# Kernel optimization log

Hardware: AMD Instinct MI355X
Metric: run time of the kernel (lower is better)

## Reference

```python
import jax, jax.numpy as jnp
import numpy as np

NUM_BANDS = 30
SPLIT_FREQ = 30
M_PARAM = 1
DIM = 2048
BATCH = 16384


def _dct_mat(N):
    # Orthonormal DCT-II matrix D: dct(x) = x @ D.T, idct(y) = y @ D
    n = np.arange(N, dtype=np.float64)
    kk = n[:, None]
    M = np.cos(np.pi * (n + 0.5) * kk / N)
    s = np.full(N, np.sqrt(2.0 / N))
    s[0] = np.sqrt(1.0 / N)
    return jnp.asarray((M * s[:, None]).astype(np.float32))


def _band_scale(freq_weights, k, N):
    # Precompute the per-frequency scale vector the torch loop applies band-by-band.
    pts = np.linspace(0, N - 1, NUM_BANDS + 1).astype(np.int64)  # torch .long() truncation
    scale = jnp.ones((N,), dtype=freq_weights.dtype)
    for i in range(NUM_BANDS):
        s, e = int(pts[i]), int(pts[i + 1])
        if e <= SPLIT_FREQ:
            f = 1.0 + freq_weights[i] * k * (1.0 - i / NUM_BANDS)
        else:
            f = 1.0 - freq_weights[i] * k * (1.0 - (i - NUM_BANDS // M_PARAM) / NUM_BANDS)
        scale = scale.at[s:e].set(f)  # bands are disjoint; base is 1
    return scale


def setup_inputs() -> dict:
    key = jax.random.key(0)
    ks = jax.random.split(key, 6)
    g = 0.02  # small init like xavier_uniform with gain 0.5
    return {
        "x": jax.random.normal(ks[0], (BATCH, DIM), dtype=jnp.float32),
        "freq_weights": jnp.ones((NUM_BANDS,), dtype=jnp.float32),
        "k": jnp.float32(0.3),
        "W1": jax.random.normal(ks[1], (1024, DIM), dtype=jnp.float32) * g,
        "b1": jnp.zeros((1024,), dtype=jnp.float32),
        "W2": jax.random.normal(ks[2], (512, 1024), dtype=jnp.float32) * g,
        "b2": jnp.zeros((512,), dtype=jnp.float32),
        "Wmu": jax.random.normal(ks[3], (256, 512), dtype=jnp.float32) * g,
        "bmu": jnp.zeros((256,), dtype=jnp.float32),
        "Wlv": jax.random.normal(ks[4], (256, 512), dtype=jnp.float32) * g,
        "blv": jnp.zeros((256,), dtype=jnp.float32),
    }


def reference(x, freq_weights, k, W1, b1, W2, b2, Wmu, bmu, Wlv, blv):
    N = x.shape[-1]
    D = _dct_mat(N)
    # DCT -> per-band reweight -> IDCT, fused as two matmuls and one vector multiply
    xd = (x @ D.T) * _band_scale(freq_weights, k, N)
    xe = xd @ D
    h = jax.nn.relu(xe @ W1.T + b1)
    h = jax.nn.relu(h @ W2.T + b2)
    mu = h @ Wmu.T + bmu
    logvar = h @ Wlv.T + blv
    return (mu, logvar)
```

## Files before the change

### kernel.cpp

```cpp
#include <hip/hip_runtime.h>
#include <hip/hip_bf16.h>
#include <math.h>

#define DIM 2048
#define BATCH 16384

typedef __attribute__((ext_vector_type(8))) short short8;
typedef __attribute__((ext_vector_type(4))) short short4v;
typedef __attribute__((ext_vector_type(4))) float floatx4;
typedef unsigned short ushort_t;

__device__ __forceinline__ ushort_t f2bf(float f) {
    union { float f; unsigned u; } v; v.f = f;
    unsigned r = v.u + 0x7FFFu + ((v.u >> 16) & 1u);
    return (ushort_t)(r >> 16);
}

__global__ void k_scale(const float* __restrict__ fw, const float* __restrict__ kp,
                        float* __restrict__ s) {
    int n = blockIdx.x * blockDim.x + threadIdx.x;
    if (n >= DIM) return;
    float kv = kp[0];
    float f = 1.0f;
    for (int i = 0; i < 30; ++i) {
        long s0 = (long)((double)i       * (double)(DIM - 1) / 30.0);
        long e0 = (long)((double)(i + 1) * (double)(DIM - 1) / 30.0);
        if (n >= s0 && n < e0) {
            if (e0 <= 30)
                f = 1.0f + fw[i] * kv * (1.0f - (float)i / 30.0f);
            else
                f = 1.0f - fw[i] * kv * (1.0f - (float)(i - 30) / 30.0f);
        }
    }
    s[n] = f;
}

__global__ void k_gen_d(ushort_t* __restrict__ D, ushort_t* __restrict__ Dt) {
    int idx = blockIdx.x * blockDim.x + threadIdx.x;
    int r = idx >> 11;
    int c = idx & (DIM - 1);
    const float w  = 7.6699039394282058e-4f;
    const float s0 = 0.02209708691207961f;
    const float s1 = 0.03125f;
    int m1 = ((2 * c + 1) * r) & (4 * DIM - 1);
    int m2 = ((2 * r + 1) * c) & (4 * DIM - 1);
    float v1 = __cosf(w * (float)m1) * (r == 0 ? s0 : s1);
    float v2 = __cosf(w * (float)m2) * (c == 0 ? s0 : s1);
    D[idx]  = f2bf(v1);
    Dt[idx] = f2bf(v2);
}

#define U_W1   262144
#define U_W2    65536
#define U_WH    16384
__global__ void k_cast_w(const float* __restrict__ W1, const float* __restrict__ W2,
                         const float* __restrict__ Wmu, const float* __restrict__ Wlv,
                         ushort_t* __restrict__ W1bf, ushort_t* __restrict__ W2bf,
                         ushort_t* __restrict__ Wcat) {
    int i = blockIdx.x * blockDim.x + threadIdx.x;
    const float* src; ushort_t* dst; int u;
    if (i < U_W1)                    { src = W1;  dst = W1bf;             u = i; }
    else if (i < U_W1 + U_W2)        { src = W2;  dst = W2bf;             u = i - U_W1; }
    else if (i < U_W1 + U_W2 + U_WH) { src = Wmu; dst = Wcat;             u = i - U_W1 - U_W2; }
    else                             { src = Wlv; dst = Wcat + 8 * U_WH;  u = i - U_W1 - U_W2 - U_WH; }
    const float4* p = reinterpret_cast<const float4*>(src) + 2 * (size_t)u;
    float4 a = p[0], b = p[1];
    short8 r;
    r[0] = (short)f2bf(a.x); r[1] = (short)f2bf(a.y);
    r[2] = (short)f2bf(a.z); r[3] = (short)f2bf(a.w);
    r[4] = (short)f2bf(b.x); r[5] = (short)f2bf(b.y);
    r[6] = (short)f2bf(b.z); r[7] = (short)f2bf(b.w);
    *reinterpret_cast<short8*>(dst + 8 * (size_t)u) = r;
}

__global__ void k_red(const float* __restrict__ P, ushort_t* __restrict__ out,
                      const float* __restrict__ scale, int n4, int n4row) {
    int i = blockIdx.x * blockDim.x + threadIdx.x;
    const float4* p = reinterpret_cast<const float4*>(P);
    float4 a = p[i], b = p[i + n4], c = p[i + 2 * n4], d = p[i + 3 * n4];
    float4 s;
    s.x = a.x + b.x + c.x + d.x;
    s.y = a.y + b.y + c.y + d.y;
    s.z = a.z + b.z + c.z + d.z;
    s.w = a.w + b.w + c.w + d.w;
    if (scale) {
        float4 sc = reinterpret_cast<const float4*>(scale)[i & (n4row - 1)];
        s.x *= sc.x; s.y *= sc.y; s.z *= sc.z; s.w *= sc.w;
    }
    short4v o;
    o[0] = (short)f2bf(s.x); o[1] = (short)f2bf(s.y);
    o[2] = (short)f2bf(s.z); o[3] = (short)f2bf(s.w);
    *reinterpret_cast<short4v*>(out + 4 * (size_t)i) = o;
}

template<int TM, int TN, int BK, int EPI, bool SK4>
__device__ __forceinline__ void gemm_core(
        const ushort_t* __restrict__ A, const ushort_t* __restrict__ B,
        ushort_t* __restrict__ Cb, float* __restrict__ Cf,
        const float* __restrict__ ep0, const float* __restrict__ ep1,
        int M, int N, int K, int KC) {
    constexpr int BM = 32 * TM;
    constexpr int BN = 32 * TN;
    constexpr int SEGS = BK / 8;
    constexpr int RSH  = (BK == 32) ? 1 : 0;
    constexpr int SSH  = (SEGS == 4) ? 2 : 3;
    __shared__ __align__(16) ushort_t As[BM * BK];
    __shared__ __align__(16) ushort_t Bs[BN * BK];

    const int tid  = threadIdx.x;
    const int lane = tid & 63;
    const int wave = tid >> 6;
    const int wm   = wave >> 1;
    const int wn   = wave & 1;
    const int q    = lane >> 4;
    const int l16  = lane & 15;

    const int tilesM = M / BM;
    const int tilesN = N / BN;
    int bid = (int)blockIdx.x;
    int sk = 0;
    if constexpr (SK4) { int nt = tilesM * tilesN; sk = bid / nt; bid = bid % nt; }
    const int xcd = bid & 7;
    const int j   = bid >> 3;
    const int bm  = xcd * (tilesM >> 3) + j / tilesN;
    const int bn  = j % tilesN;

    floatx4 acc[TM][TN];
    #pragma unroll
    for (int i = 0; i < TM; ++i)
        #pragma unroll
        for (int jj = 0; jj < TN; ++jj)
            acc[i][jj] = (floatx4){0.f, 0.f, 0.f, 0.f};

    const long aBase = (long)bm * BM * K + (long)sk * KC;
    const long bBase = (long)bn * BN * K + (long)sk * KC;
    const int  KLOOP = SK4 ? KC : K;

    for (int kt = 0; kt < KLOOP; kt += BK) {
        __syncthreads();
        #pragma unroll
        for (int i = 0; i < BM * BK / 2048; ++i) {
            int idx = tid + i * 256;
            int row = idx >> SSH, seg = idx & (SEGS - 1);
            int gseg = seg ^ ((row >> RSH) & (SEGS - 1));
            const ushort_t* g = A + aBase + (long)row * K + kt + gseg * 8;
            __builtin_amdgcn_global_load_lds(
                (const __attribute__((address_space(1))) void*)g,
                (__attribute__((address_space(3))) void*)(As + idx * 8),
                16, 0, 0);
        }
        #pragma unroll
        for (int i = 0; i < BN * BK / 2048; ++i) {
            int idx = tid + i * 256;
            int row = idx >> SSH, seg = idx & (SEGS - 1);
            int gseg = seg ^ ((row >> RSH) & (SEGS - 1));
            const ushort_t* g = B + bBase + (long)row * K + kt + gseg * 8;
            __builtin_amdgcn_global_load_lds(
                (const __attribute__((address_space(1))) void*)g,
                (__attribute__((address_space(3))) void*)(Bs + idx * 8),
                16, 0, 0);
        }
        __syncthreads();

        #pragma unroll
        for (int ks = 0; ks < BK / 32; ++ks) {
            short8 af[TM], bfr[TN];
            #pragma unroll
            for (int t = 0; t < TM; ++t) {
                int srow = wm * TM * 16 + t * 16 + l16;
                int rseg = (ks * 4 + q) ^ ((srow >> RSH) & (SEGS - 1));
                af[t] = *reinterpret_cast<const short8*>(&As[srow * BK + rseg * 8]);
            }
            #pragma unroll
            for (int t = 0; t < TN; ++t) {
                int srow = wn * TN * 16 + t * 16 + l16;
                int rseg = (ks * 4 + q) ^ ((srow >> RSH) & (SEGS - 1));
                bfr[t] = *reinterpret_cast<const short8*>(&Bs[srow * BK + rseg * 8]);
            }
            #pragma unroll
            for (int i = 0; i < TM; ++i)
                #pragma unroll
                for (int jj = 0; jj < TN; ++jj)
                    acc[i][jj] = __builtin_amdgcn_mfma_f32_16x16x32_bf16(
                        af[i], bfr[jj], acc[i][jj], 0, 0, 0);
        }
    }

    #pragma unroll
    for (int i = 0; i < TM; ++i) {
        #pragma unroll
        for (int jj = 0; jj < TN; ++jj) {
            #pragma unroll
            for (int r = 0; r < 4; ++r) {
                int row = bm * BM + wm * TM * 16 + i * 16 + q * 4 + r;
                int col = bn * BN + wn * TN * 16 + jj * 16 + l16;
                float v = acc[i][jj][r];
                if constexpr (EPI == 2) {
                    v += ep0[col];
                    v = v > 0.f ? v : 0.f;
                    Cb[(long)row * N + col] = f2bf(v);
                } else if constexpr (EPI == 3) {
                    const int half = N >> 1;
                    if (col < half)
                        Cf[(long)row * half + col] = v + ep0[col];
                    else
                        Cf[(long)M * half + (long)row * half + (col - half)] = v + ep1[col - half];
                } else {
                    Cf[(long)sk * M * N + (long)row * N + col] = v;
                }
            }
        }
    }
}

__global__ __launch_bounds__(512, 2) void g2f(const float* __restrict__ Xf,
        const ushort_t* __restrict__ B, ushort_t* __restrict__ Cb,
        const float* __restrict__ bias, int M, int N, int K) {
    constexpr int BM = 256, BN = 256, BK = 32;
    __shared__ __align__(16) ushort_t As[4][BM * BK];
    __shared__ __align__(16) ushort_t Bs[4][BN * BK];

    const int tid  = threadIdx.x;
    const int lane = tid & 63;
    const int wave = tid >> 6;
    const int wm   = wave >> 2;
    const int wn   = wave & 3;
    const int q    = lane >> 4;
    const int l16  = lane & 15;

    const int tilesM = M / BM;
    const int tilesN = N / BN;
    int bid = (int)blockIdx.x;
    const int xcd = bid & 7;
    const int jb  = bid >> 3;
    const int bm  = xcd * (tilesM >> 3) + jb / tilesN;
    const int bn  = jb % tilesN;
    const int NT  = K / BK;

    const long aBase = (long)bm * BM * K;
    const long bBase = (long)bn * BN * K;

    floatx4 acc[8][4];
    #pragma unroll
    for (int i = 0; i < 8; ++i)
        #pragma unroll
        for (int j = 0; j < 4; ++j)
            acc[i][j] = (floatx4){0.f, 0.f, 0.f, 0.f};

    float4 rAa[4], rAb[4];

#define LDA(tt, RA) do {                                                            \
        _Pragma("unroll")                                                           \
        for (int _g = 0; _g < 2; ++_g) {                                            \
            int _idx = _g * 512 + tid;                                              \
            int _row = _idx >> 2, _seg = _idx & 3;                                  \
            int _gs = _seg ^ ((_row >> 1) & 3);                                     \
            const float4* _p = reinterpret_cast<const float4*>(                     \
                Xf + aBase + (long)_row * K + (tt) * BK + _gs * 8);                 \
            RA[2 * _g]     = _p[0];                                                 \
            RA[2 * _g + 1] = _p[1];                                                 \
        } } while (0)

#define CVW(tt, RA) do { const int _sl = (tt) & 3;                                  \
        _Pragma("unroll")                                                           \
        for (int _g = 0; _g < 2; ++_g) {                                            \
            int _idx = _g * 512 + tid;                                              \
            float4 _a = RA[2 * _g], _b = RA[2 * _g + 1];                            \
            short8 _o;                                                              \
            _o[0] = (short)f2bf(_a.x); _o[1] = (short)f2bf(_a.y);                   \
            _o[2] = (short)f2bf(_a.z); _o[3] = (short)f2bf(_a.w);                   \
            _o[4] = (short)f2bf(_b.x); _o[5] = (short)f2bf(_b.y);                   \
            _o[6] = (short)f2bf(_b.z); _o[7] = (short)f2bf(_b.w);                   \
            *reinterpret_cast<short8*>(&As[_sl][_idx * 8]) = _o;                    \
        } } while (0)

#define STG_B(tt) do { const int _sl = (tt) & 3;                                    \
        _Pragma("unroll")                                                           \
        for (int _g = 0; _g < 2; ++_g) {                                            \
            int _idx = _g * 512 + tid;                                              \
            int _row = _idx >> 2, _seg = _idx & 3;                                  \
            int _gs = _seg ^ ((_row >> 1) & 3);                                     \
            const ushort_t* _gp = B + bBase + (long)_row * K + (tt) * BK + _gs * 8; \
            __builtin_amdgcn_global_load_lds(                                       \
                (const __attribute__((address_space(1))) void*)_gp,                 \
                (__attribute__((address_space(3))) void*)(&Bs[_sl][_idx * 8]),      \
                16, 0, 0);                                                          \
        } } while (0)

#define ITER(tt, RA) do {                                                           \
        const int _slot = (tt) & 3;                                                 \
        if ((tt) + 2 < NT) CVW((tt) + 2, RA);                                       \
        short8 _bf[4], _alo[4], _ahi[4];                                            \
        _Pragma("unroll")                                                           \
        for (int _j = 0; _j < 4; ++_j) {                                            \
            int _sr = wn * 64 + _j * 16 + l16;                                      \
            int _rs = q ^ ((_sr >> 1) & 3);                                         \
            _bf[_j] = *reinterpret_cast<const short8*>(&Bs[_slot][_sr * BK + _rs * 8]); \
        }                                                                           \
        _Pragma("unroll")                                                           \
        for (int _i = 0; _i < 4; ++_i) {                                            \
            int _sr = wm * 128 + _i * 16 + l16;                                     \
            int _rs = q ^ ((_sr >> 1) & 3);                                         \
            _alo[_i] = *reinterpret_cast<const short8*>(&As[_slot][_sr * BK + _rs * 8]); \
        }                                                                           \
        _Pragma("unroll")                                                           \
        for (int _i = 0; _i < 4; ++_i) {                                            \
            int _sr = wm * 128 + 64 + _i * 16 + l16;                                \
            int _rs = q ^ ((_sr >> 1) & 3);                                         \
            _ahi[_i] = *reinterpret_cast<const short8*>(&As[_slot][_sr * BK + _rs * 8]); \
        }                                                                           \
        if ((tt) + 3 < NT) STG_B((tt) + 3);                                         \
        if ((tt) + 4 < NT) LDA((tt) + 4, RA);                                       \
        __builtin_amdgcn_s_setprio(1);                                              \
        _Pragma("unroll")                                                           \
        for (int _i = 0; _i < 4; ++_i)                                              \
            _Pragma("unroll")                                                       \
            for (int _j = 0; _j < 4; ++_j)                                          \
                acc[_i][_j] = __builtin_amdgcn_mfma_f32_16x16x32_bf16(              \
                    _alo[_i], _bf[_j], acc[_i][_j], 0, 0, 0);                       \
        _Pragma("unroll")                                                           \
        for (int _i = 0; _i < 4; ++_i)                                              \
            _Pragma("unroll")                                                       \
            for (int _j = 0; _j < 4; ++_j)                                          \
                acc[4 + _i][_j] = __builtin_amdgcn_mfma_f32_16x16x32_bf16(          \
                    _ahi[_i], _bf[_j], acc[4 + _i][_j], 0, 0, 0);                   \
        __builtin_amdgcn_s_setprio(0);                                              \
        asm volatile("s_waitcnt lgkmcnt(0)" ::: "memory");                          \
        __builtin_amdgcn_sched_barrier(0);                                          \
        if ((tt) == NT - 2)                                                         \
            asm volatile("s_waitcnt vmcnt(0)" ::: "memory");                        \
        __builtin_amdgcn_s_barrier();                                               \
        asm volatile("" ::: "memory");                                              \
    } while (0)

    LDA(0, rAa); CVW(0, rAa);
    LDA(1, rAb); CVW(1, rAb);
    LDA(2, rAa); LDA(3, rAb);
    STG_B(0); STG_B(1); STG_B(2);
    asm volatile("s_waitcnt lgkmcnt(0)" ::: "memory");
    asm volatile("s_waitcnt vmcnt(4)" ::: "memory");
    __builtin_amdgcn_s_barrier();
    asm volatile("" ::: "memory");

    for (int t = 0; t < NT; t += 2) {
        ITER(t, rAa);
        ITER(t + 1, rAb);
    }

#undef ITER
#undef STG_B
#undef CVW
#undef LDA

    float bsv[4];
    #pragma unroll
    for (int j = 0; j < 4; ++j)
        bsv[j] = bias[bn * BN + wn * 64 + j * 16 + l16];
    #pragma unroll
    for (int i = 0; i < 8; ++i) {
        int row = bm * BM + wm * 128 + i * 16 + q * 4;
        #pragma unroll
        for (int j = 0; j < 4; ++j) {
            int col = bn * BN + wn * 64 + j * 16 + l16;
            #pragma unroll
            for (int r = 0; r < 4; ++r) {
                float v = acc[i][j][r] + bsv[j];
                v = v > 0.f ? v : 0.f;
                Cb[(long)(row + r) * N + col] = f2bf(v);
            }
        }
    }
}

template<int EPI>
__device__ __forceinline__ void gemm128_v2(
        const ushort_t* __restrict__ A, const ushort_t* __restrict__ B,
        ushort_t* __restrict__ Cb, float* __restrict__ Cf,
        const float* __restrict__ ep0, const float* __restrict__ ep1,
        int M, int N, int K) {
    constexpr int BM = 128, BN = 128, BK = 32;
    __shared__ __align__(16) ushort_t As[4][BM * BK];
    __shared__ __align__(16) ushort_t Bs[4][BN * BK];

    const int tid  = threadIdx.x;
    const int lane = tid & 63;
    const int wave = tid >> 6;
    const int wm   = wave >> 1;
    const int wn   = wave & 1;
    const int q    = lane >> 4;
    const int l16  = lane & 15;

    const int tilesM = M / BM;
    const int tilesN = N / BN;
    int bid = (int)blockIdx.x;
    const int xcd = bid & 7;
    const int jb  = bid >> 3;
    const int bm  = xcd * (tilesM >> 3) + jb / tilesN;
    const int bn  = jb % tilesN;
    const int NT  = K / BK;

    const long aBase = (long)bm * BM * K;
    const long bBase = (long)bn * BN * K;

    floatx4 acc[4][4];
    #pragma unroll
    for (int i = 0; i < 4; ++i)
        #pragma unroll
        for (int j = 0; j < 4; ++j)
            acc[i][j] = (floatx4){0.f, 0.f, 0.f, 0.f};

#define STAGE_A(t) do { int _sl = (t) & 3;                                          \
        _Pragma("unroll")                                                           \
        for (int _g = 0; _g < 2; ++_g) {                                            \
            int _idx = _g * 256 + tid;                                              \
            int _row = _idx >> 2, _seg = _idx & 3;                                  \
            int _gs = _seg ^ ((_row >> 1) & 3);                                     \
            const ushort_t* _gp = A + aBase + (long)_row * K + (t) * BK + _gs * 8;  \
            __builtin_amdgcn_global_load_lds(                                       \
                (const __attribute__((address_space(1))) void*)_gp,                 \
                (__attribute__((address_space(3))) void*)(&As[_sl][_idx * 8]),      \
                16, 0, 0);                                                          \
        } } while (0)
#define STAGE_B(t) do { int _sl = (t) & 3;                                          \
        _Pragma("unroll")                                                           \
        for (int _g = 0; _g < 2; ++_g) {                                            \
            int _idx = _g * 256 + tid;                                              \
            int _row = _idx >> 2, _seg = _idx & 3;                                  \
            int _gs = _seg ^ ((_row >> 1) & 3);                                     \
            const ushort_t* _gp = B + bBase + (long)_row * K + (t) * BK + _gs * 8;  \
            __builtin_amdgcn_global_load_lds(                                       \
                (const __attribute__((address_space(1))) void*)_gp,                 \
                (__attribute__((address_space(3))) void*)(&Bs[_sl][_idx * 8]),      \
                16, 0, 0);                                                          \
        } } while (0)

    STAGE_A(0); STAGE_B(0);
    STAGE_A(1); STAGE_B(1);
    STAGE_A(2); STAGE_B(2);
    asm volatile("s_waitcnt vmcnt(8)" ::: "memory");
    __builtin_amdgcn_s_barrier();
    asm volatile("" ::: "memory");

#define KTILE(tt, DOSTAGE, WAITOP) do {                                             \
        const int _slot = (tt) & 3;                                                 \
        short8 _bf[4], _af[4];                                                      \
        _Pragma("unroll")                                                           \
        for (int _j = 0; _j < 4; ++_j) {                                            \
            int _sr = wn * 64 + _j * 16 + l16;                                      \
            int _rs = q ^ ((_sr >> 1) & 3);                                         \
            _bf[_j] = *reinterpret_cast<const short8*>(&Bs[_slot][_sr * BK + _rs * 8]); \
        }                                                                           \
        _Pragma("unroll")                                                           \
        for (int _i = 0; _i < 4; ++_i) {                                            \
            int _sr = wm * 64 + _i * 16 + l16;                                      \
            int _rs = q ^ ((_sr >> 1) & 3);                                         \
            _af[_i] = *reinterpret_cast<const short8*>(&As[_slot][_sr * BK + _rs * 8]); \
        }                                                                           \
        if (DOSTAGE) { STAGE_A((tt) + 3); STAGE_B((tt) + 3); }                      \
        __builtin_amdgcn_s_setprio(1);                                              \
        _Pragma("unroll")                                                           \
        for (int _i = 0; _i < 4; ++_i)                                              \
            _Pragma("unroll")                                                       \
            for (int _j = 0; _j < 4; ++_j)                                          \
                acc[_i][_j] = __builtin_amdgcn_mfma_f32_16x16x32_bf16(              \
                    _af[_i], _bf[_j], acc[_i][_j], 0, 0, 0);                        \
        __builtin_amdgcn_s_setprio(0);                                              \
        asm volatile("s_waitcnt lgkmcnt(0)" ::: "memory");                          \
        __builtin_amdgcn_sched_barrier(0);                                          \
        WAITOP;                                                                     \
        __builtin_amdgcn_s_barrier();                                               \
        asm volatile("" ::: "memory");                                              \
    } while (0)

    int t = 0;
    for (; t < NT - 3; ++t) {
        KTILE(t, true, asm volatile("s_waitcnt vmcnt(8)" ::: "memory"));
    }
    KTILE(t, false, asm volatile("s_waitcnt vmcnt(4)" ::: "memory")); ++t;
    KTILE(t, false, asm volatile("s_waitcnt vmcnt(0)" ::: "memory")); ++t;
    KTILE(t, false, (void)0);

#undef KTILE
#undef STAGE_A
#undef STAGE_B

    #pragma unroll
    for (int i = 0; i < 4; ++i) {
        #pragma unroll
        for (int jj = 0; jj < 4; ++jj) {
            #pragma unroll
            for (int r = 0; r < 4; ++r) {
                int row = bm * BM + wm * 64 + i * 16 + q * 4 + r;
                int col = bn * BN + wn * 64 + jj * 16 + l16;
                float v = acc[i][jj][r];
                if constexpr (EPI == 2) {
                    v += ep0[col];
                    v = v > 0.f ? v : 0.f;
                    Cb[(long)row * N + col] = f2bf(v);
                } else {
                    const int half = N >> 1;
                    v += (col < half) ? ep0[col] : ep1[col - half];
                    if (col < half)
                        Cf[(long)row * half + col] = v;
                    else
                        Cf[(long)M * half + (long)row * half + (col - half)] = v;
                }
            }
        }
    }
}

__global__ __launch_bounds__(256) void g0p_sk(const ushort_t* A, const ushort_t* B,
        float* P, int M, int N, int K, int KC) {
    gemm_core<4, 4, 32, 4, true>(A, B, nullptr, P, nullptr, nullptr, M, N, K, KC);
}
__global__ __launch_bounds__(256) void g1p_sk(const ushort_t* A, const ushort_t* B,
        float* P, int M, int N, int K, int KC) {
    gemm_core<4, 4, 32, 4, true>(A, B, nullptr, P, nullptr, nullptr, M, N, K, KC);
}
__global__ __launch_bounds__(256, 2) void g3_h2(const ushort_t* A, const ushort_t* B,
        ushort_t* Cb, const float* ep0, int M, int N, int K) {
    gemm128_v2<2>(A, B, Cb, nullptr, ep0, nullptr, M, N, K);
}
__global__ __launch_bounds__(256, 2) void g4_head(const ushort_t* A, const ushort_t* B,
        float* Cf, const float* ep0, const float* ep1, int M, int N, int K) {
    gemm128_v2<3>(A, B, nullptr, Cf, ep0, ep1, M, N, K);
}

extern "C" void kernel_launch(void* const* d_in, const int* in_sizes, int n_in,
                              void* d_out, int out_size, void* d_ws, size_t ws_size,
                              hipStream_t stream) {
    const float* x   = (const float*)d_in[0];
    const float* fw  = (const float*)d_in[1];
    const float* kp  = (const float*)d_in[2];
    const float* W1  = (const float*)d_in[3];
    const float* b1  = (const float*)d_in[4];
    const float* W2  = (const float*)d_in[5];
    const float* b2  = (const float*)d_in[6];
    const float* Wmu = (const float*)d_in[7];
    const float* bmu = (const float*)d_in[8];
    const float* Wlv = (const float*)d_in[9];
    const float* blv = (const float*)d_in[10];
    float* out = (float*)d_out;

    char* ws = (char*)d_ws;
    const size_t MB = 1024 * 1024;
    ushort_t* W1bf = (ushort_t*)(ws + 0);
    ushort_t* Dbf  = (ushort_t*)(ws + 4   * MB);
    ushort_t* Dtbf = (ushort_t*)(ws + 12  * MB);
    ushort_t* T1sT = (ushort_t*)(ws + 20  * MB);
    ushort_t* H1   = (ushort_t*)(ws + 0);
    float*    P    = (float*)   (ws + 32  * MB);
    ushort_t* H2   = (ushort_t*)(ws + 96  * MB);
    ushort_t* M1T  = (ushort_t*)(ws + 112 * MB);
    ushort_t* W2bf = (ushort_t*)(ws + 116 * MB);
    ushort_t* Wcat = (ushort_t*)(ws + 117 * MB);
    float*    svec = (float*)   (ws + 118 * MB);

    hipLaunchKernelGGL(k_scale, dim3(DIM / 256), dim3(256), 0, stream, fw, kp, svec);
    hipLaunchKernelGGL(k_gen_d, dim3(DIM * DIM / 256), dim3(256), 0, stream, Dbf, Dtbf);
    hipLaunchKernelGGL(k_cast_w, dim3((U_W1 + U_W2 + 2 * U_WH) / 256), dim3(256), 0, stream,
                       W1, W2, Wmu, Wlv, W1bf, W2bf, Wcat);

    hipLaunchKernelGGL(g0p_sk, dim3(8 * 16 * 4), dim3(256), 0, stream,
                       W1bf, Dbf, P, 1024, 2048, 2048, 512);
    hipLaunchKernelGGL(k_red, dim3(1024 * 2048 / 4 / 256), dim3(256), 0, stream,
                       P, T1sT, svec, 1024 * 2048 / 4, 2048 / 4);
    hipLaunchKernelGGL(g1p_sk, dim3(8 * 16 * 4), dim3(256), 0, stream,
                       T1sT, Dtbf, P, 1024, 2048, 2048, 512);
    hipLaunchKernelGGL(k_red, dim3(1024 * 2048 / 4 / 256), dim3(256), 0, stream,
                       P, M1T, nullptr, 1024 * 2048 / 4, 2048 / 4);

    hipLaunchKernelGGL(g2f, dim3((BATCH / 256) * (1024 / 256)), dim3(512), 0, stream,
                       x, M1T, H1, b1, BATCH, 1024, 2048);
    hipLaunchKernelGGL(g3_h2, dim3((BATCH / 128) * (512 / 128)), dim3(256), 0, stream,
                       H1, W2bf, H2, b2, BATCH, 512, 1024);
    hipLaunchKernelGGL(g4_head, dim3((BATCH / 128) * (512 / 128)), dim3(256), 0, stream,
                       H2, Wcat, out, bmu, blv, BATCH, 512, 512);

    (void)in_sizes; (void)n_in; (void)out_size; (void)ws_size;
}
```

Measured before the change: 376.6 us.

## Use 4-stage pipelined GEMM for split-K DCT GEMMs and merge prep kernels

Replaces the single-buffered gemm_core used by the split-K DCT-fold GEMMs with the 4-slot, 3-tile-ahead prefetching gemm128 pipeline. That pipeline uses explicit vmcnt waits and setprio, and it is generalized to support split-K. The two split-K GEMMs now carry launch_bounds(256,2). The three setup kernels (scale, DCT matrix generation, weight cast) are merged into one launch to cut launch overhead. A k_cast_x kernel is added but never launched. The 4-slot buffers raise LDS use per block.

```diff
diff --git a/kernel.cpp b/kernel.cpp
--- a/kernel.cpp
+++ b/kernel.cpp
@@ -16,61 +16,77 @@
     return (ushort_t)(r >> 16);
 }
 
-__global__ void k_scale(const float* __restrict__ fw, const float* __restrict__ kp,
-                        float* __restrict__ s) {
-    int n = blockIdx.x * blockDim.x + threadIdx.x;
-    if (n >= DIM) return;
-    float kv = kp[0];
-    float f = 1.0f;
-    for (int i = 0; i < 30; ++i) {
-        long s0 = (long)((double)i       * (double)(DIM - 1) / 30.0);
-        long e0 = (long)((double)(i + 1) * (double)(DIM - 1) / 30.0);
-        if (n >= s0 && n < e0) {
-            if (e0 <= 30)
-                f = 1.0f + fw[i] * kv * (1.0f - (float)i / 30.0f);
-            else
-                f = 1.0f - fw[i] * kv * (1.0f - (float)(i - 30) / 30.0f);
-        }
-    }
-    s[n] = f;
-}
-
-__global__ void k_gen_d(ushort_t* __restrict__ D, ushort_t* __restrict__ Dt) {
-    int idx = blockIdx.x * blockDim.x + threadIdx.x;
-    int r = idx >> 11;
-    int c = idx & (DIM - 1);
-    const float w  = 7.6699039394282058e-4f;
-    const float s0 = 0.02209708691207961f;
-    const float s1 = 0.03125f;
-    int m1 = ((2 * c + 1) * r) & (4 * DIM - 1);
-    int m2 = ((2 * r + 1) * c) & (4 * DIM - 1);
-    float v1 = __cosf(w * (float)m1) * (r == 0 ? s0 : s1);
-    float v2 = __cosf(w * (float)m2) * (c == 0 ? s0 : s1);
-    D[idx]  = f2bf(v1);
-    Dt[idx] = f2bf(v2);
-}
-
 #define U_W1   262144
 #define U_W2    65536
 #define U_WH    16384
-__global__ void k_cast_w(const float* __restrict__ W1, const float* __restrict__ W2,
-                         const float* __restrict__ Wmu, const float* __restrict__ Wlv,
-                         ushort_t* __restrict__ W1bf, ushort_t* __restrict__ W2bf,
-                         ushort_t* __restrict__ Wcat) {
+#define NB_GEND  (DIM * DIM / 256)
+#define NB_CASTW ((U_W1 + U_W2 + 2 * U_WH) / 256)
+__global__ void k_prep(const float* __restrict__ fw, const float* __restrict__ kp,
+                       float* __restrict__ s,
+                       ushort_t* __restrict__ D, ushort_t* __restrict__ Dt,
+                       const float* __restrict__ W1, const float* __restrict__ W2,
+                       const float* __restrict__ Wmu, const float* __restrict__ Wlv,
+                       ushort_t* __restrict__ W1bf, ushort_t* __restrict__ W2bf,
+                       ushort_t* __restrict__ Wcat) {
+    int b = blockIdx.x;
+    if (b < NB_GEND) {
+        int idx = b * 256 + threadIdx.x;
+        int r = idx >> 11;
+        int c = idx & (DIM - 1);
+        const float w  = 7.6699039394282058e-4f;
+        const float s0 = 0.02209708691207961f;
+        const float s1 = 0.03125f;
+        int m1 = ((2 * c + 1) * r) & (4 * DIM - 1);
+        int m2 = ((2 * r + 1) * c) & (4 * DIM - 1);
+        float v1 = __cosf(w * (float)m1) * (r == 0 ? s0 : s1);
+        float v2 = __cosf(w * (float)m2) * (c == 0 ? s0 : s1);
+        D[idx]  = f2bf(v1);
+        Dt[idx] = f2bf(v2);
+    } else if (b < NB_GEND + NB_CASTW) {
+        int i = (b - NB_GEND) * 256 + threadIdx.x;
+        const float* src; ushort_t* dst; int u;
+        if (i < U_W1)                    { src = W1;  dst = W1bf;             u = i; }
+        else if (i < U_W1 + U_W2)        { src = W2;  dst = W2bf;             u = i - U_W1; }
+        else if (i < U_W1 + U_W2 + U_WH) { src = Wmu; dst = Wcat;             u = i - U_W1 - U_W2; }
+        else                             { src = Wlv; dst = Wcat + 8 * U_WH;  u = i - U_W1 - U_W2 - U_WH; }
+        const float4* p = reinterpret_cast<const float4*>(src) + 2 * (size_t)u;
+        float4 a = p[0], bb = p[1];
+        short8 r;
+        r[0] = (short)f2bf(a.x);  r[1] = (short)f2bf(a.y);
+        r[2] = (short)f2bf(a.z);  r[3] = (short)f2bf(a.w);
+        r[4] = (short)f2bf(bb.x); r[5] = (short)f2bf(bb.y);
+        r[6] = (short)f2bf(bb.z); r[7] = (short)f2bf(bb.w);
+        *reinterpret_cast<short8*>(dst + 8 * (size_t)u) = r;
+    } else {
+        int n = (b - NB_GEND - NB_CASTW) * 256 + threadIdx.x;
+        if (n < DIM) {
+            float kv = kp[0];
+            float f = 1.0f;
+            for (int i = 0; i < 30; ++i) {
+                long s0 = (long)((double)i       * (double)(DIM - 1) / 30.0);
+                long e0 = (long)((double)(i + 1) * (double)(DIM - 1) / 30.0);
+                if (n >= s0 && n < e0) {
+                    if (e0 <= 30)
+                        f = 1.0f + fw[i] * kv * (1.0f - (float)i / 30.0f);
+                    else
+                        f = 1.0f - fw[i] * kv * (1.0f - (float)(i - 30) / 30.0f);
+                }
+            }
+            s[n] = f;
+        }
+    }
+}
+
+__global__ void k_cast_x(const float* __restrict__ in, ushort_t* __restrict__ out) {
     int i = blockIdx.x * blockDim.x + threadIdx.x;
-    const float* src; ushort_t* dst; int u;
-    if (i < U_W1)                    { src = W1;  dst = W1bf;             u = i; }
-    else if (i < U_W1 + U_W2)        { src = W2;  dst = W2bf;             u = i - U_W1; }
-    else if (i < U_W1 + U_W2 + U_WH) { src = Wmu; dst = Wcat;             u = i - U_W1 - U_W2; }
-    else                             { src = Wlv; dst = Wcat + 8 * U_WH;  u = i - U_W1 - U_W2 - U_WH; }
-    const float4* p = reinterpret_cast<const float4*>(src) + 2 * (size_t)u;
+    const float4* p = reinterpret_cast<const float4*>(in) + 2 * (size_t)i;
     float4 a = p[0], b = p[1];
     short8 r;
     r[0] = (short)f2bf(a.x); r[1] = (short)f2bf(a.y);
     r[2] = (short)f2bf(a.z); r[3] = (short)f2bf(a.w);
     r[4] = (short)f2bf(b.x); r[5] = (short)f2bf(b.y);
     r[6] = (short)f2bf(b.z); r[7] = (short)f2bf(b.w);
-    *reinterpret_cast<short8*>(dst + 8 * (size_t)u) = r;
+    *reinterpret_cast<short8*>(out + 8 * (size_t)i) = r;
 }
 
 __global__ void k_red(const float* __restrict__ P, ushort_t* __restrict__ out,
@@ -93,19 +109,15 @@
     *reinterpret_cast<short4v*>(out + 4 * (size_t)i) = o;
 }
 
-template<int TM, int TN, int BK, int EPI, bool SK4>
-__device__ __forceinline__ void gemm_core(
+template<int EPI, bool SK4>
+__device__ __forceinline__ void gemm128p(
         const ushort_t* __restrict__ A, const ushort_t* __restrict__ B,
         ushort_t* __restrict__ Cb, float* __restrict__ Cf,
         const float* __restrict__ ep0, const float* __restrict__ ep1,
         int M, int N, int K, int KC) {
-    constexpr int BM = 32 * TM;
-    constexpr int BN = 32 * TN;
-    constexpr int SEGS = BK / 8;
-    constexpr int RSH  = (BK == 32) ? 1 : 0;
-    constexpr int SSH  = (SEGS == 4) ? 2 : 3;
-    __shared__ __align__(16) ushort_t As[BM * BK];
-    __shared__ __align__(16) ushort_t Bs[BN * BK];
+    constexpr int BM = 128, BN = 128, BK = 32;
+    __shared__ __align__(16) ushort_t As[4][BM * BK];
+    __shared__ __align__(16) ushort_t Bs[4][BN * BK];
 
     const int tid  = threadIdx.x;
     const int lane = tid & 63;
@@ -121,79 +133,104 @@
     int sk = 0;
     if constexpr (SK4) { int nt = tilesM * tilesN; sk = bid / nt; bid = bid % nt; }
     const int xcd = bid & 7;
-    const int j   = bid >> 3;
-    const int bm  = xcd * (tilesM >> 3) + j / tilesN;
-    const int bn  = j % tilesN;
-
-    floatx4 acc[TM][TN];
-    #pragma unroll
-    for (int i = 0; i < TM; ++i)
-        #pragma unroll
-        for (int jj = 0; jj < TN; ++jj)
-            acc[i][jj] = (floatx4){0.f, 0.f, 0.f, 0.f};
+    const int jb  = bid >> 3;
+    const int bm  = xcd * (tilesM >> 3) + jb / tilesN;
+    const int bn  = jb % tilesN;
+    const int NT  = (SK4 ? KC : K) / BK;
 
     const long aBase = (long)bm * BM * K + (long)sk * KC;
     const long bBase = (long)bn * BN * K + (long)sk * KC;
-    const int  KLOOP = SK4 ? KC : K;
-
-    for (int kt = 0; kt < KLOOP; kt += BK) {
-        __syncthreads();
+
+    floatx4 acc[4][4];
+    #pragma unroll
+    for (int i = 0; i < 4; ++i)
         #pragma unroll
-        for (int i = 0; i < BM * BK / 2048; ++i) {
-            int idx = tid + i * 256;
-            int row = idx >> SSH, seg = idx & (SEGS - 1);
-            int gseg = seg ^ ((row >> RSH) & (SEGS - 1));
-            const ushort_t* g = A + aBase + (long)row * K + kt + gseg * 8;
-            __builtin_amdgcn_global_load_lds(
-                (const __attribute__((address_space(1))) void*)g,
-                (__attribute__((address_space(3))) void*)(As + idx * 8),
-                16, 0, 0);
-        }
+        for (int j = 0; j < 4; ++j)
+            acc[i][j] = (floatx4){0.f, 0.f, 0.f, 0.f};
+
+#define STAGE_A(t) do { int _sl = (t) & 3;                                          \
+        _Pragma("unroll")                                                           \
+        for (int _g = 0; _g < 2; ++_g) {                                            \
+            int _idx = _g * 256 + tid;                                              \
+            int _row = _idx >> 2, _seg = _idx & 3;                                  \
+            int _gs = _seg ^ ((_row >> 1) & 3);                                     \
+            const ushort_t* _gp = A + aBase + (long)_row * K + (t) * BK + _gs * 8;  \
+            __builtin_amdgcn_global_load_lds(                                       \
+                (const __attribute__((address_space(1))) void*)_gp,                 \
+                (__attribute__((address_space(3))) void*)(&As[_sl][_idx * 8]),      \
+                16, 0, 0);                                                          \
+        } } while (0)
+#define STAGE_B(t) do { int _sl = (t) & 3;                                          \
+        _Pragma("unroll")                                                           \
+        for (int _g = 0; _g < 2; ++_g) {                                            \
+            int _idx = _g * 256 + tid;                                              \
+            int _row = _idx >> 2, _seg = _idx & 3;                                  \
+            int _gs = _seg ^ ((_row >> 1) & 3);                                     \
+            const ushort_t* _gp = B + bBase + (long)_row * K + (t) * BK + _gs * 8;  \
+            __builtin_amdgcn_global_load_lds(                                       \
+                (const __attribute__((address_space(1))) void*)_gp,                 \
+                (__attribute__((address_space(3))) void*)(&Bs[_sl][_idx * 8]),      \
+                16, 0, 0);                                                          \
+        } } while (0)
+
+    STAGE_A(0); STAGE_B(0);
+    STAGE_A(1); STAGE_B(1);
+    STAGE_A(2); STAGE_B(2);
+    asm volatile("s_waitcnt vmcnt(8)" ::: "memory");
+    __builtin_amdgcn_s_barrier();
+    asm volatile("" ::: "memory");
+
+#define KTILE(tt, DOSTAGE, WAITOP) do {                                             \
+        const int _slot = (tt) & 3;                                                 \
+        short8 _bf[4], _af[4];                                                      \
+        _Pragma("unroll")                                                           \
+        for (int _j = 0; _j < 4; ++_j) {                                            \
+            int _sr = wn * 64 + _j * 16 + l16;                                      \
+            int _rs = q ^ ((_sr >> 1) & 3);                                         \
+            _bf[_j] = *reinterpret_cast<const short8*>(&Bs[_slot][_sr * BK + _rs * 8]); \
+        }                                                                           \
+        _Pragma("unroll")                                                           \
+        for (int _i = 0; _i < 4; ++_i) {                                            \
+            int _sr = wm * 64 + _i * 16 + l16;                                      \
+            int _rs = q ^ ((_sr >> 1) & 3);                                         \
+            _af[_i] = *reinterpret_cast<const short8*>(&As[_slot][_sr * BK + _rs * 8]); \
+        }                                                                           \
+        if (DOSTAGE) { STAGE_A((tt) + 3); STAGE_B((tt) + 3); }                      \
+        __builtin_amdgcn_s_setprio(1);                                              \
+        _Pragma("unroll")                                                           \
+        for (int _i = 0; _i < 4; ++_i)                                              \
+            _Pragma("unroll")                                                       \
+            for (int _j = 0; _j < 4; ++_j)                                          \
+                acc[_i][_j] = __builtin_amdgcn_mfma_f32_16x16x32_bf16(              \
+                    _af[_i], _bf[_j], acc[_i][_j], 0, 0, 0);                        \
+        __builtin_amdgcn_s_setprio(0);                                              \
+        asm volatile("s_waitcnt lgkmcnt(0)" ::: "memory");                          \
+        __builtin_amdgcn_sched_barrier(0);                                          \
+        WAITOP;                                                                     \
+        __builtin_amdgcn_s_barrier();                                               \
+        asm volatile("" ::: "memory");                                              \
+    } while (0)
+
+    int t = 0;
+    for (; t < NT - 3; ++t) {
+        KTILE(t, true, asm volatile("s_waitcnt vmcnt(8)" ::: "memory"));
+    }
+    KTILE(t, false, asm volatile("s_waitcnt vmcnt(4)" ::: "memory")); ++t;
+    KTILE(t, false, asm volatile("s_waitcnt vmcnt(0)" ::: "memory")); ++t;
+    KTILE(t, false, (void)0);
+
+#undef KTILE
+#undef STAGE_A
+#undef STAGE_B
+
+    #pragma unroll
+    for (int i = 0; i < 4; ++i) {
         #pragma unroll
-        for (int i = 0; i < BN * BK / 2048; ++i) {
-            int idx = tid + i * 256;
-            int row = idx >> SSH, seg = idx & (SEGS - 1);
-            int gseg = seg ^ ((row >> RSH) & (SEGS - 1));
-            const ushort_t* g = B + bBase + (long)row * K + kt + gseg * 8;
-            __builtin_amdgcn_global_load_lds(
-                (const __attribute__((address_space(1))) void*)g,
-                (__attribute__((address_space(3))) void*)(Bs + idx * 8),
-                16, 0, 0);
-        }
-        __syncthreads();
-
-        #pragma unroll
-        for (int ks = 0; ks < BK / 32; ++ks) {
-            short8 af[TM], bfr[TN];
-            #pragma unroll
-            for (int t = 0; t < TM; ++t) {
-                int srow = wm * TM * 16 + t * 16 + l16;
-                int rseg = (ks * 4 + q) ^ ((srow >> RSH) & (SEGS - 1));
-                af[t] = *reinterpret_cast<const short8*>(&As[srow * BK + rseg * 8]);
-            }
-            #pragma unroll
-            for (int t = 0; t < TN; ++t) {
-                int srow = wn * TN * 16 + t * 16 + l16;
-                int rseg = (ks * 4 + q) ^ ((srow >> RSH) & (SEGS - 1));
-                bfr[t] = *reinterpret_cast<const short8*>(&Bs[srow * BK + rseg * 8]);
-            }
-            #pragma unroll
-            for (int i = 0; i < TM; ++i)
-                #pragma unroll
-                for (int jj = 0; jj < TN; ++jj)
-                    acc[i][jj] = __builtin_amdgcn_mfma_f32_16x16x32_bf16(
-                        af[i], bfr[jj], acc[i][jj], 0, 0, 0);
-        }
-    }
-
-    #pragma unroll
-    for (int i = 0; i < TM; ++i) {
-        #pragma unroll
-        for (int jj = 0; jj < TN; ++jj) {
+        for (int jj = 0; jj < 4; ++jj) {
             #pragma unroll
             for (int r = 0; r < 4; ++r) {
-                int row = bm * BM + wm * TM * 16 + i * 16 + q * 4 + r;
-                int col = bn * BN + wn * TN * 16 + jj * 16 + l16;
+                int row = bm * BM + wm * 64 + i * 16 + q * 4 + r;
+                int col = bn * BN + wn * 64 + jj * 16 + l16;
                 float v = acc[i][jj][r];
                 if constexpr (EPI == 2) {
                     v += ep0[col];
@@ -201,10 +238,11 @@
                     Cb[(long)row * N + col] = f2bf(v);
                 } else if constexpr (EPI == 3) {
                     const int half = N >> 1;
+                    v += (col < half) ? ep0[col] : ep1[col - half];
                     if (col < half)
-                        Cf[(long)row * half + col] = v + ep0[col];
+                        Cf[(long)row * half + col] = v;
                     else
-                        Cf[(long)M * half + (long)row * half + (col - half)] = v + ep1[col - half];
+                        Cf[(long)M * half + (long)row * half + (col - half)] = v;
                 } else {
                     Cf[(long)sk * M * N + (long)row * N + col] = v;
                 }
@@ -372,159 +410,21 @@
     }
 }
 
-template<int EPI>
-__device__ __forceinline__ void gemm128_v2(
-        const ushort_t* __restrict__ A, const ushort_t* __restrict__ B,
-        ushort_t* __restrict__ Cb, float* __restrict__ Cf,
-        const float* __restrict__ ep0, const float* __restrict__ ep1,
-        int M, int N, int K) {
-    constexpr int BM = 128, BN = 128, BK = 32;
-    __shared__ __align__(16) ushort_t As[4][BM * BK];
-    __shared__ __align__(16) ushort_t Bs[4][BN * BK];
-
-    const int tid  = threadIdx.x;
-    const int lane = tid & 63;
-    const int wave = tid >> 6;
-    const int wm   = wave >> 1;
-    const int wn   = wave & 1;
-    const int q    = lane >> 4;
-    const int l16  = lane & 15;
-
-    const int tilesM = M / BM;
-    const int tilesN = N / BN;
-    int bid = (int)blockIdx.x;
-    const int xcd = bid & 7;
-    const int jb  = bid >> 3;
-    const int bm  = xcd * (tilesM >> 3) + jb / tilesN;
-    const int bn  = jb % tilesN;
-    const int NT  = K / BK;
-
-    const long aBase = (long)bm * BM * K;
-    const long bBase = (long)bn * BN * K;
-
-    floatx4 acc[4][4];
-    #pragma unroll
-    for (int i = 0; i < 4; ++i)
-        #pragma unroll
-        for (int j = 0; j < 4; ++j)
-            acc[i][j] = (floatx4){0.f, 0.f, 0.f, 0.f};
-
-#define STAGE_A(t) do { int _sl = (t) & 3;                                          \
-        _Pragma("unroll")                                                           \
-        for (int _g = 0; _g < 2; ++_g) {                                            \
-            int _idx = _g * 256 + tid;                                              \
-            int _row = _idx >> 2, _seg = _idx & 3;                                  \
-            int _gs = _seg ^ ((_row >> 1) & 3);                                     \
-            const ushort_t* _gp = A + aBase + (long)_row * K + (t) * BK + _gs * 8;  \
-            __builtin_amdgcn_global_load_lds(                                       \
-                (const __attribute__((address_space(1))) void*)_gp,                 \
-                (__attribute__((address_space(3))) void*)(&As[_sl][_idx * 8]),      \
-                16, 0, 0);                                                          \
-        } } while (0)
-#define STAGE_B(t) do { int _sl = (t) & 3;                                          \
-        _Pragma("unroll")                                                           \
-        for (int _g = 0; _g < 2; ++_g) {                                            \
-            int _idx = _g * 256 + tid;                                              \
-            int _row = _idx >> 2, _seg = _idx & 3;                                  \
-            int _gs = _seg ^ ((_row >> 1) & 3);                                     \
-            const ushort_t* _gp = B + bBase + (long)_row * K + (t) * BK + _gs * 8;  \
-            __builtin_amdgcn_global_load_lds(                                       \
-                (const __attribute__((address_space(1))) void*)_gp,                 \
-                (__attribute__((address_space(3))) void*)(&Bs[_sl][_idx * 8]),      \
-                16, 0, 0);                                                          \
-        } } while (0)
-
-    STAGE_A(0); STAGE_B(0);
-    STAGE_A(1); STAGE_B(1);
-    STAGE_A(2); STAGE_B(2);
-    asm volatile("s_waitcnt vmcnt(8)" ::: "memory");
-    __builtin_amdgcn_s_barrier();
-    asm volatile("" ::: "memory");
-
-#define KTILE(tt, DOSTAGE, WAITOP) do {                                             \
-        const int _slot = (tt) & 3;                                                 \
-        short8 _bf[4], _af[4];                                                      \
-        _Pragma("unroll")                                                           \
-        for (int _j = 0; _j < 4; ++_j) {                                            \
-            int _sr = wn * 64 + _j * 16 + l16;                                      \
-            int _rs = q ^ ((_sr >> 1) & 3);                                         \
-            _bf[_j] = *reinterpret_cast<const short8*>(&Bs[_slot][_sr * BK + _rs * 8]); \
-        }                                                                           \
-        _Pragma("unroll")                                                           \
-        for (int _i = 0; _i < 4; ++_i) {                                            \
-            int _sr = wm * 64 + _i * 16 + l16;                                      \
-            int _rs = q ^ ((_sr >> 1) & 3);                                         \
-            _af[_i] = *reinterpret_cast<const short8*>(&As[_slot][_sr * BK + _rs * 8]); \
-        }                                                                           \
-        if (DOSTAGE) { STAGE_A((tt) + 3); STAGE_B((tt) + 3); }                      \
-        __builtin_amdgcn_s_setprio(1);                                              \
-        _Pragma("unroll")                                                           \
-        for (int _i = 0; _i < 4; ++_i)                                              \
-            _Pragma("unroll")                                                       \
-            for (int _j = 0; _j < 4; ++_j)                                          \
-                acc[_i][_j] = __builtin_amdgcn_mfma_f32_16x16x32_bf16(              \
-                    _af[_i], _bf[_j], acc[_i][_j], 0, 0, 0);                        \
-        __builtin_amdgcn_s_setprio(0);                                              \
-        asm volatile("s_waitcnt lgkmcnt(0)" ::: "memory");                          \
-        __builtin_amdgcn_sched_barrier(0);                                          \
-        WAITOP;                                                                     \
-        __builtin_amdgcn_s_barrier();                                               \
-        asm volatile("" ::: "memory");                                              \
-    } while (0)
-
-    int t = 0;
-    for (; t < NT - 3; ++t) {
-        KTILE(t, true, asm volatile("s_waitcnt vmcnt(8)" ::: "memory"));
-    }
-    KTILE(t, false, asm volatile("s_waitcnt vmcnt(4)" ::: "memory")); ++t;
-    KTILE(t, false, asm volatile("s_waitcnt vmcnt(0)" ::: "memory")); ++t;
-    KTILE(t, false, (void)0);
-
-#undef KTILE
-#undef STAGE_A
-#undef STAGE_B
-
-    #pragma unroll
-    for (int i = 0; i < 4; ++i) {
-        #pragma unroll
-        for (int jj = 0; jj < 4; ++jj) {
-            #pragma unroll
-            for (int r = 0; r < 4; ++r) {
-                int row = bm * BM + wm * 64 + i * 16 + q * 4 + r;
-                int col = bn * BN + wn * 64 + jj * 16 + l16;
-                float v = acc[i][jj][r];
-                if constexpr (EPI == 2) {
-                    v += ep0[col];
-                    v = v > 0.f ? v : 0.f;
-                    Cb[(long)row * N + col] = f2bf(v);
-                } else {
-                    const int half = N >> 1;
-                    v += (col < half) ? ep0[col] : ep1[col - half];
-                    if (col < half)
-                        Cf[(long)row * half + col] = v;
-                    else
-                        Cf[(long)M * half + (long)row * half + (col - half)] = v;
-                }
-            }
-        }
-    }
-}
-
-__global__ __launch_bounds__(256) void g0p_sk(const ushort_t* A, const ushort_t* B,
+__global__ __launch_bounds__(256, 2) void g0p_sk(const ushort_t* A, const ushort_t* B,
         float* P, int M, int N, int K, int KC) {
-    gemm_core<4, 4, 32, 4, true>(A, B, nullptr, P, nullptr, nullptr, M, N, K, KC);
-}
-__global__ __launch_bounds__(256) void g1p_sk(const ushort_t* A, const ushort_t* B,
+    gemm128p<4, true>(A, B, nullptr, P, nullptr, nullptr, M, N, K, KC);
+}
+__global__ __launch_bounds__(256, 2) void g1p_sk(const ushort_t* A, const ushort_t* B,
         float* P, int M, int N, int K, int KC) {
-    gemm_core<4, 4, 32, 4, true>(A, B, nullptr, P, nullptr, nullptr, M, N, K, KC);
+    gemm128p<4, true>(A, B, nullptr, P, nullptr, nullptr, M, N, K, KC);
 }
 __global__ __launch_bounds__(256, 2) void g3_h2(const ushort_t* A, const ushort_t* B,
         ushort_t* Cb, const float* ep0, int M, int N, int K) {
-    gemm128_v2<2>(A, B, Cb, nullptr, ep0, nullptr, M, N, K);
+    gemm128p<2, false>(A, B, Cb, nullptr, ep0, nullptr, M, N, K, 0);
 }
 __global__ __launch_bounds__(256, 2) void g4_head(const ushort_t* A, const ushort_t* B,
         float* Cf, const float* ep0, const float* ep1, int M, int N, int K) {
-    gemm128_v2<3>(A, B, nullptr, Cf, ep0, ep1, M, N, K);
+    gemm128p<3, false>(A, B, nullptr, Cf, ep0, ep1, M, N, K, 0);
 }
 
 extern "C" void kernel_launch(void* const* d_in, const int* in_sizes, int n_in,
@@ -557,10 +457,8 @@
     ushort_t* Wcat = (ushort_t*)(ws + 117 * MB);
     float*    svec = (float*)   (ws + 118 * MB);
 
-    hipLaunchKernelGGL(k_scale, dim3(DIM / 256), dim3(256), 0, stream, fw, kp, svec);
-    hipLaunchKernelGGL(k_gen_d, dim3(DIM * DIM / 256), dim3(256), 0, stream, Dbf, Dtbf);
-    hipLaunchKernelGGL(k_cast_w, dim3((U_W1 + U_W2 + 2 * U_WH) / 256), dim3(256), 0, stream,
-                       W1, W2, Wmu, Wlv, W1bf, W2bf, Wcat);
+    hipLaunchKernelGGL(k_prep, dim3(NB_GEND + NB_CASTW + DIM / 256), dim3(256), 0, stream,
+                       fw, kp, svec, Dbf, Dtbf, W1, W2, Wmu, Wlv, W1bf, W2bf, Wcat);
 
     hipLaunchKernelGGL(g0p_sk, dim3(8 * 16 * 4), dim3(256), 0, stream,
                        W1bf, Dbf, P, 1024, 2048, 2048, 512);
```

Result: faster. 364.4 us (-3.3%).
